# Performance work log

Measured on AMD Instinct MI355X. Metric: run time of the kernel, lower is better.

## Reference

```python
import jax, jax.numpy as jnp
import numpy as np

N, E, B = 20000, 320000, 128      # nodes, edges, graphs in batch
H = 32                            # h_atom == n_bond
N_ATOM_FEAT, N_BOND_FEAT = 64, 16
N_LAYERS = 2


def setup_inputs() -> dict:
    key = jax.random.key(0)
    ks = jax.random.split(key, 12)
    s = 0.1
    return dict(
        n_feat=jax.random.normal(ks[0], (N, N_ATOM_FEAT), jnp.float32),
        e_feat=jax.random.normal(ks[1], (E, N_BOND_FEAT), jnp.float32),
        src=jax.random.randint(ks[2], (E,), 0, N, jnp.int32),
        dst=jax.random.randint(ks[3], (E,), 0, N, jnp.int32),
        graph_ids=jnp.sort(jax.random.randint(ks[4], (N,), 0, B, jnp.int32)),
        W_atom=jax.random.normal(ks[5], (N_ATOM_FEAT, H), jnp.float32) * s,
        b_atom=jnp.zeros((H,), jnp.float32),
        W_bond=jax.random.normal(ks[6], (N_BOND_FEAT, H), jnp.float32) * s,
        b_bond=jnp.zeros((H,), jnp.float32),
        W_e1=jax.random.normal(ks[7], (H, H), jnp.float32) * s,
        b_e1=jnp.zeros((H,), jnp.float32),
        W_e2=jax.random.normal(ks[8], (H, H * H), jnp.float32) * s,
        b_e2=jnp.zeros((H * H,), jnp.float32),
        W_ih=jax.random.normal(ks[9], (3 * H, H), jnp.float32) * s,
        W_hh=jax.random.normal(ks[10], (3 * H, H), jnp.float32) * s,
        b_ih=jnp.zeros((3 * H,), jnp.float32),
        b_hh=jnp.zeros((3 * H,), jnp.float32),
    )


def _gru_step(x, h, W_ih, W_hh, b_ih, b_hh):
    # torch nn.GRU single-cell update (seq_len=1)
    gi = x @ W_ih.T + b_ih
    gh = h @ W_hh.T + b_hh
    ir, iz, ig = jnp.split(gi, 3, axis=-1)
    hr, hz, hg = jnp.split(gh, 3, axis=-1)
    r = jax.nn.sigmoid(ir + hr)
    z = jax.nn.sigmoid(iz + hz)
    n = jnp.tanh(ig + r * hg)
    return (1.0 - z) * n + z * h


def reference(n_feat, e_feat, src, dst, graph_ids, W_atom, b_atom, W_bond, b_bond,
              W_e1, b_e1, W_e2, b_e2, W_ih, W_hh, b_ih, b_hh):
    # dense embeddings
    h = n_feat @ W_atom + b_atom              # [N, H]
    h_bond = e_feat @ W_bond + b_bond         # [E, H]
    # NNConv edge network -> per-edge weight matrix [E, H_in, H_out]
    ew = jax.nn.relu(h_bond @ W_e1 + b_e1) @ W_e2 + b_e2
    W_edge = ew.reshape(E, H, H)
    # in-degree for mean aggregation (zero in-degree -> 0, like DGL mean)
    deg = jax.ops.segment_sum(jnp.ones((E,), h.dtype), dst, num_segments=N)
    inv_deg = 1.0 / jnp.maximum(deg, 1.0)
    for _ in range(N_LAYERS):
        msg = jnp.einsum('ei,eio->eo', h[src], W_edge)                  # [E, H]
        agg = jax.ops.segment_sum(msg, dst, num_segments=N) * inv_deg[:, None]
        m = jax.nn.relu(agg)
        h = _gru_step(m, h, W_ih, W_hh, b_ih, b_hh)
    # dgl.mean_nodes: per-graph mean of node states
    gsum = jax.ops.segment_sum(h, graph_ids, num_segments=B)            # [B, H]
    gcnt = jax.ops.segment_sum(jnp.ones((N,), h.dtype), graph_ids, num_segments=B)
    return gsum / jnp.maximum(gcnt, 1.0)[:, None]
```

## Files before the change

kernel.cpp:

```cpp
#include <hip/hip_runtime.h>
#include <hip/hip_fp16.h>
#include <math.h>

#define N_NODES 20000
#define N_EDGES 320000
#define NB 128
#define H 32
#define AF 64
#define BF 16
#define SCB 79
#define SCP 20224
#define EMB_BLOCKS 2500
#define PACK_BLOCKS 66
#define ZERO_BLOCKS 16

typedef _Float16 f16x2 __attribute__((ext_vector_type(2)));

__device__ __forceinline__ float fast_sigmoid(float x) {
  return 1.0f / (1.0f + __expf(-x));
}
__device__ __forceinline__ float fast_tanh(float x) {
  float e2 = __expf(2.0f * x);
  return 1.0f - 2.0f / (e2 + 1.0f);
}
__device__ __forceinline__ unsigned int pk2(float a, float b) {
  union { f16x2 h; unsigned int u; } p;
  p.h[0] = (_Float16)a;
  p.h[1] = (_Float16)b;
  return p.u;
}
__device__ __forceinline__ float uph(unsigned int u, int hi) {
  union { unsigned int u; f16x2 h; } x; x.u = u;
  return hi ? (float)x.h[1] : (float)x.h[0];
}
__device__ __forceinline__ float dot2(unsigned int a, unsigned int b, float c) {
  union { unsigned int u; f16x2 h; } ua, ub;
  ua.u = a; ub.u = b;
#if __has_builtin(__builtin_amdgcn_fdot2)
  return __builtin_amdgcn_fdot2(ua.h, ub.h, c, false);
#else
  return c + (float)ua.h[0] * (float)ub.h[0] + (float)ua.h[1] * (float)ub.h[1];
#endif
}

__global__ __launch_bounds__(256) void prep(const float* __restrict__ nf,
    const float* __restrict__ W, const float* __restrict__ b, float* __restrict__ h,
    const float* __restrict__ We2, const float* __restrict__ be2,
    unsigned int* __restrict__ Wp, int* __restrict__ hist2buf) {
  int blk = blockIdx.x;
  int tid = threadIdx.x;
  if (blk < EMB_BLOCKS) {
    __shared__ float Ws[AF * H];
    __shared__ float nfs[8][AF];
    for (int v = tid; v < AF * H; v += 256) Ws[v] = W[v];
    int n0 = blk * 8;
    for (int v = tid; v < 8 * AF; v += 256) {
      int nl = v / AF, k = v % AF;
      nfs[nl][k] = nf[(size_t)(n0 + nl) * AF + k];
    }
    __syncthreads();
    int nl = tid / H, o = tid % H;
    int n = n0 + nl;
    float acc = b[o];
#pragma unroll
    for (int k = 0; k < AF; k++) acc += nfs[nl][k] * Ws[k * H + o];
    h[(size_t)n * H + o] = acc;
  } else if (blk < EMB_BLOCKS + PACK_BLOCKS) {
    int idx = (blk - EMB_BLOCKS) * 256 + tid;
    if (idx < 33 * 512) {
      int j = idx >> 9, r = idx & 511;
      int ip = r >> 5, o = r & 31;
      const float* src = (j < 32) ? (We2 + (size_t)j * (H * H)) : be2;
      Wp[idx] = pk2(src[(2 * ip) * H + o], src[(2 * ip + 1) * H + o]);
    }
  } else {
    int idx = (blk - EMB_BLOCKS - PACK_BLOCKS) * 256 + tid;
    for (int i = idx; i < 2 * N_NODES; i += ZERO_BLOCKS * 256) hist2buf[i] = 0;
  }
}

__global__ void hist2(const int* __restrict__ src, const int* __restrict__ dst,
                      int* __restrict__ hsrc, int* __restrict__ hdst) {
  int e = blockIdx.x * 256 + threadIdx.x;
  if (e < N_EDGES) {
    atomicAdd(&hsrc[src[e]], 1);
    atomicAdd(&hdst[dst[e]], 1);
  }
}

__global__ __launch_bounds__(256) void scan_partial(const int* __restrict__ hist_s,
    const int* __restrict__ hist_d, int* __restrict__ part, int* __restrict__ bsum) {
  __shared__ int wsums[4];
  int which = blockIdx.y;
  const int* __restrict__ hh = which ? hist_d : hist_s;
  int i = blockIdx.x * 256 + threadIdx.x;
  int v = (i < N_NODES) ? hh[i] : 0;
  int lane = threadIdx.x & 63, wid = threadIdx.x >> 6;
  int incl = v;
#pragma unroll
  for (int off = 1; off < 64; off <<= 1) {
    int t = __shfl_up(incl, off, 64);
    if (lane >= off) incl += t;
  }
  if (lane == 63) wsums[wid] = incl;
  __syncthreads();
  int woff = 0;
#pragma unroll
  for (int w = 0; w < 4; w++) if (w < wid) woff += wsums[w];
  part[which * SCP + i] = woff + incl - v;
  if (threadIdx.x == 0)
    bsum[which * SCB + blockIdx.x] = wsums[0] + wsums[1] + wsums[2] + wsums[3];
}

__global__ __launch_bounds__(256) void scan_tops(int* __restrict__ bsum,
    const int* __restrict__ gid, int* __restrict__ gstart) {
  __shared__ int s[2 * SCB];
  int tid = threadIdx.x;
  if (tid < 2 * SCB) s[tid] = bsum[tid];
  if (tid < NB) {
    int g = tid;
    int lo = 0, hi = N_NODES;
    while (lo < hi) { int mid = (lo + hi) >> 1; if (gid[mid] < g) lo = mid + 1; else hi = mid; }
    gstart[g] = lo;
    if (g == 0) gstart[NB] = N_NODES;
  }
  __syncthreads();
  if (tid < 2) {
    int run = 0;
    for (int b = 0; b < SCB; b++) { int t = s[tid * SCB + b]; s[tid * SCB + b] = run; run += t; }
  }
  __syncthreads();
  if (tid < 2 * SCB) bsum[tid] = s[tid];
}

__global__ __launch_bounds__(256) void scan_final(const int* __restrict__ part,
    const int* __restrict__ bsum, const int* __restrict__ hist_d,
    int* __restrict__ cur_s, int* __restrict__ cur_d,
    int* __restrict__ seg_s, int* __restrict__ seg_d, float* __restrict__ inv_deg) {
  int which = blockIdx.y;
  int i = blockIdx.x * 256 + threadIdx.x;
  if (i >= N_NODES) return;
  int ex = part[which * SCP + i] + bsum[which * SCB + blockIdx.x];
  if (which == 0) {
    cur_s[i] = ex; seg_s[i] = ex;
    if (i == 0) seg_s[N_NODES] = N_EDGES;
  } else {
    cur_d[i] = ex; seg_d[i] = ex;
    inv_deg[i] = 1.0f / fmaxf((float)hist_d[i], 1.0f);
    if (i == 0) seg_d[N_NODES] = N_EDGES;
  }
}

__global__ void scatter2_full(const int* __restrict__ src, const int* __restrict__ dst,
    int* __restrict__ cur_s, int* __restrict__ cur_d,
    int* __restrict__ src_s, int* __restrict__ dst_s,
    int* __restrict__ pos_s, int* __restrict__ dpos) {
  int e = blockIdx.x * 256 + threadIdx.x;
  if (e >= N_EDGES) return;
  int s = src[e], d = dst[e];
  int ps = atomicAdd(&cur_s[s], 1);
  int pd = atomicAdd(&cur_d[d], 1);
  src_s[ps] = s;
  dst_s[ps] = d;
  dpos[ps] = pd;
  pos_s[e] = ps;
}

__device__ __forceinline__ uint2 edge_r_core(const float* __restrict__ ef,
    const float* __restrict__ Wb, const float* __restrict__ bb,
    const float* __restrict__ We1, const float* __restrict__ be1,
    float* Wbs, unsigned int* W1p, float* efs, unsigned int* hbp,
    int e0, int tid) {
  for (int v = tid; v < BF * H; v += 256) Wbs[v] = Wb[v];
  for (int v = tid; v < 16 * H; v += 256) {
    int jp = v >> 5, o = v & 31;
    W1p[v] = pk2(We1[(2 * jp) * H + o], We1[(2 * jp + 1) * H + o]);
  }
  if (tid < 128) {
    float4 d = ((const float4*)(ef + (size_t)e0 * BF))[tid];
    ((float4*)(efs + (tid >> 2) * 20))[tid & 3] = d;
  }
  __syncthreads();
  int el = tid >> 3, oq = tid & 7;
  const float4* Wb4 = (const float4*)Wbs;
  const float4* efv = (const float4*)(efs + el * 20);
  float4 hb = ((const float4*)bb)[oq];
#pragma unroll
  for (int kq = 0; kq < 4; kq++) {
    float4 e4 = efv[kq];
    float4 w;
    w = Wb4[(kq * 4 + 0) * 8 + oq];
    hb.x += e4.x * w.x; hb.y += e4.x * w.y; hb.z += e4.x * w.z; hb.w += e4.x * w.w;
    w = Wb4[(kq * 4 + 1) * 8 + oq];
    hb.x += e4.y * w.x; hb.y += e4.y * w.y; hb.z += e4.y * w.z; hb.w += e4.y * w.w;
    w = Wb4[(kq * 4 + 2) * 8 + oq];
    hb.x += e4.z * w.x; hb.y += e4.z * w.y; hb.z += e4.z * w.z; hb.w += e4.z * w.w;
    w = Wb4[(kq * 4 + 3) * 8 + oq];
    hb.x += e4.w * w.x; hb.y += e4.w * w.y; hb.z += e4.w * w.z; hb.w += e4.w * w.w;
  }
  ((uint2*)(hbp + el * 20))[oq] = make_uint2(pk2(hb.x, hb.y), pk2(hb.z, hb.w));
  __syncthreads();
  float4 acc = ((const float4*)be1)[oq];
  const uint4* hb4 = (const uint4*)(hbp + el * 20);
#pragma unroll
  for (int q = 0; q < 4; q++) {
    uint4 hp = hb4[q];
    uint4 w;
    w = ((const uint4*)(W1p + (4 * q + 0) * H))[oq];
    acc.x = dot2(hp.x, w.x, acc.x); acc.y = dot2(hp.x, w.y, acc.y);
    acc.z = dot2(hp.x, w.z, acc.z); acc.w = dot2(hp.x, w.w, acc.w);
    w = ((const uint4*)(W1p + (4 * q + 1) * H))[oq];
    acc.x = dot2(hp.y, w.x, acc.x); acc.y = dot2(hp.y, w.y, acc.y);
    acc.z = dot2(hp.y, w.z, acc.z); acc.w = dot2(hp.y, w.w, acc.w);
    w = ((const uint4*)(W1p + (4 * q + 2) * H))[oq];
    acc.x = dot2(hp.z, w.x, acc.x); acc.y = dot2(hp.z, w.y, acc.y);
    acc.z = dot2(hp.z, w.z, acc.z); acc.w = dot2(hp.z, w.w, acc.w);
    w = ((const uint4*)(W1p + (4 * q + 3) * H))[oq];
    acc.x = dot2(hp.w, w.x, acc.x); acc.y = dot2(hp.w, w.y, acc.y);
    acc.z = dot2(hp.w, w.z, acc.z); acc.w = dot2(hp.w, w.w, acc.w);
  }
  acc.x = fmaxf(acc.x, 0.0f); acc.y = fmaxf(acc.y, 0.0f);
  acc.z = fmaxf(acc.z, 0.0f); acc.w = fmaxf(acc.w, 0.0f);
  uint2 st;
  st.x = pk2(acc.x, acc.y);
  st.y = pk2(acc.z, acc.w);
  return st;
}

__global__ __launch_bounds__(256) void edge_r_scatter(const float* __restrict__ ef,
    const float* __restrict__ Wb, const float* __restrict__ bb,
    const float* __restrict__ We1, const float* __restrict__ be1,
    const int* __restrict__ src, const int* __restrict__ dst,
    int* __restrict__ cur_s, int* __restrict__ cur_d,
    int* __restrict__ dpos, unsigned int* __restrict__ rh) {
  __shared__ float Wbs[BF * H];
  __shared__ unsigned int W1p[16 * H];
  __shared__ float efs[32 * 20];
  __shared__ unsigned int hbp[32 * 20];
  __shared__ int psh[32];
  int tid = threadIdx.x;
  int e0 = blockIdx.x * 32;
  int ps0 = 0, pd0 = 0;
  if (tid < 32) {
    int e = e0 + tid;
    int s = src[e], d = dst[e];
    ps0 = atomicAdd(&cur_s[s], 1);
    pd0 = atomicAdd(&cur_d[d], 1);
  }
  for (int v = tid; v < BF * H; v += 256) Wbs[v] = Wb[v];
  for (int v = tid; v < 16 * H; v += 256) {
    int jp = v >> 5, o = v & 31;
    W1p[v] = pk2(We1[(2 * jp) * H + o], We1[(2 * jp + 1) * H + o]);
  }
  if (tid < 128) {
    float4 d = ((const float4*)(ef + (size_t)e0 * BF))[tid];
    ((float4*)(efs + (tid >> 2) * 20))[tid & 3] = d;
  }
  __syncthreads();
  int el = tid >> 3, oq = tid & 7;
  const float4* Wb4 = (const float4*)Wbs;
  const float4* efv = (const float4*)(efs + el * 20);
  float4 hb = ((const float4*)bb)[oq];
#pragma unroll
  for (int kq = 0; kq < 4; kq++) {
    float4 e4 = efv[kq];
    float4 w;
    w = Wb4[(kq * 4 + 0) * 8 + oq];
    hb.x += e4.x * w.x; hb.y += e4.x * w.y; hb.z += e4.x * w.z; hb.w += e4.x * w.w;
    w = Wb4[(kq * 4 + 1) * 8 + oq];
    hb.x += e4.y * w.x; hb.y += e4.y * w.y; hb.z += e4.y * w.z; hb.w += e4.y * w.w;
    w = Wb4[(kq * 4 + 2) * 8 + oq];
    hb.x += e4.z * w.x; hb.y += e4.z * w.y; hb.z += e4.z * w.z; hb.w += e4.z * w.w;
    w = Wb4[(kq * 4 + 3) * 8 + oq];
    hb.x += e4.w * w.x; hb.y += e4.w * w.y; hb.z += e4.w * w.z; hb.w += e4.w * w.w;
  }
  ((uint2*)(hbp + el * 20))[oq] = make_uint2(pk2(hb.x, hb.y), pk2(hb.z, hb.w));
  if (tid < 32) {
    dpos[ps0] = pd0;
    psh[tid] = ps0;
  }
  __syncthreads();
  float4 acc = ((const float4*)be1)[oq];
  const uint4* hb4 = (const uint4*)(hbp + el * 20);
#pragma unroll
  for (int q = 0; q < 4; q++) {
    uint4 hp = hb4[q];
    uint4 w;
    w = ((const uint4*)(W1p + (4 * q + 0) * H))[oq];
    acc.x = dot2(hp.x, w.x, acc.x); acc.y = dot2(hp.x, w.y, acc.y);
    acc.z = dot2(hp.x, w.z, acc.z); acc.w = dot2(hp.x, w.w, acc.w);
    w = ((const uint4*)(W1p + (4 * q + 1) * H))[oq];
    acc.x = dot2(hp.y, w.x, acc.x); acc.y = dot2(hp.y, w.y, acc.y);
    acc.z = dot2(hp.y, w.z, acc.z); acc.w = dot2(hp.y, w.w, acc.w);
    w = ((const uint4*)(W1p + (4 * q + 2) * H))[oq];
    acc.x = dot2(hp.z, w.x, acc.x); acc.y = dot2(hp.z, w.y, acc.y);
    acc.z = dot2(hp.z, w.z, acc.z); acc.w = dot2(hp.z, w.w, acc.w);
    w = ((const uint4*)(W1p + (4 * q + 3) * H))[oq];
    acc.x = dot2(hp.w, w.x, acc.x); acc.y = dot2(hp.w, w.y, acc.y);
    acc.z = dot2(hp.w, w.z, acc.z); acc.w = dot2(hp.w, w.w, acc.w);
  }
  acc.x = fmaxf(acc.x, 0.0f); acc.y = fmaxf(acc.y, 0.0f);
  acc.z = fmaxf(acc.z, 0.0f); acc.w = fmaxf(acc.w, 0.0f);
  int ps = psh[el];
  uint2 st;
  st.x = pk2(acc.x, acc.y);
  st.y = pk2(acc.z, acc.w);
  ((uint2*)(rh + (size_t)ps * 16))[oq] = st;
}

__global__ __launch_bounds__(256) void edge_r(const float* __restrict__ ef,
    const float* __restrict__ Wb, const float* __restrict__ bb,
    const float* __restrict__ We1, const float* __restrict__ be1,
    const int* __restrict__ pos_s, unsigned int* __restrict__ rh) {
  __shared__ float Wbs[BF * H];
  __shared__ unsigned int W1p[16 * H];
  __shared__ float efs[32 * 20];
  __shared__ unsigned int hbp[32 * 20];
  int tid = threadIdx.x;
  int e0 = blockIdx.x * 32;
  uint2 st = edge_r_core(ef, Wb, bb, We1, be1, Wbs, W1p, efs, hbp, e0, tid);
  int el = tid >> 3, oq = tid & 7;
  int ps = pos_s[e0 + el];
  ((uint2*)(rh + (size_t)ps * 16))[oq] = st;
}

__device__ __forceinline__ void msg_phase(const unsigned int* __restrict__ Wp,
    const unsigned int* __restrict__ rh, const int* __restrict__ dpos,
    unsigned int* __restrict__ msg_out,
    unsigned int* Ts, const unsigned int* hp, float* hb, const int* sseg, int tid) {
  {
    int jp = tid >> 4, oh = tid & 15;
    uint2 w0[16], w1[16];
    const unsigned int* W0 = Wp + (size_t)(2 * jp) * 512 + 2 * oh;
    const unsigned int* W1 = Wp + (size_t)(2 * jp + 1) * 512 + 2 * oh;
#pragma unroll
    for (int ip = 0; ip < 16; ip++) {
      w0[ip] = *(const uint2*)(W0 + ip * 32);
      w1[ip] = *(const uint2*)(W1 + ip * 32);
    }
#pragma unroll
    for (int nl = 0; nl < 8; nl++) {
      uint4 h0 = ((const uint4*)(hp + nl * 16))[0];
      uint4 h1 = ((const uint4*)(hp + nl * 16))[1];
      uint4 h2 = ((const uint4*)(hp + nl * 16))[2];
      uint4 h3 = ((const uint4*)(hp + nl * 16))[3];
      unsigned int hr[16] = {h0.x, h0.y, h0.z, h0.w, h1.x, h1.y, h1.z, h1.w,
                             h2.x, h2.y, h2.z, h2.w, h3.x, h3.y, h3.z, h3.w};
      float t00 = 0.f, t01 = 0.f, t10 = 0.f, t11 = 0.f;
#pragma unroll
      for (int ip = 0; ip < 16; ip++) {
        unsigned int hpv = hr[ip];
        t00 = dot2(hpv, w0[ip].x, t00);
        t01 = dot2(hpv, w0[ip].y, t01);
        t10 = dot2(hpv, w1[ip].x, t10);
        t11 = dot2(hpv, w1[ip].y, t11);
      }
      ((uint2*)(Ts + nl * 512 + jp * 32 + 2 * oh))[0] =
          make_uint2(pk2(t00, t10), pk2(t01, t11));
    }
  }
  {
    int nl = tid >> 5, o = tid & 31;
    const unsigned int* Wb32 = Wp + (size_t)32 * 512 + o;
    float acc = 0.f;
#pragma unroll
    for (int ip = 0; ip < 16; ip++)
      acc = dot2(hp[nl * 16 + ip], Wb32[ip * 32], acc);
    hb[nl * H + o] = acc;
  }
  __syncthreads();
  int lane = tid & 63, wid = tid >> 6;
  int el = lane >> 3, t = lane & 7;
  for (int s = 0; s < 8; s++) {
    int a = sseg[s], bnd = sseg[s + 1];
    int ww = (wid + s) & 3;
    if (a + ww * 8 >= bnd) continue;
    const unsigned int* Trow = Ts + s * 512;
    uint4 tw[16];
#pragma unroll
    for (int jp = 0; jp < 16; jp++) tw[jp] = ((const uint4*)(Trow + jp * 32))[t];
    float4 hbv = ((const float4*)(hb + s * H))[t];
    for (int base = a + ww * 8; base < bnd; base += 32) {
      int e = base + el;
      bool valid = (e < bnd);
      int pd = 0;
      unsigned int rr[16];
#pragma unroll
      for (int k = 0; k < 16; k++) rr[k] = 0u;
      if (valid) {
        pd = dpos[e];
        const uint4* rp = (const uint4*)(rh + (size_t)e * 16);
        *(uint4*)(&rr[0])  = rp[0];
        *(uint4*)(&rr[4])  = rp[1];
        *(uint4*)(&rr[8])  = rp[2];
        *(uint4*)(&rr[12]) = rp[3];
      }
      float4 acc = hbv;
#pragma unroll
      for (int jp = 0; jp < 16; jp++) {
        unsigned int rj = rr[jp];
        uint4 w = tw[jp];
        acc.x = dot2(rj, w.x, acc.x);
        acc.y = dot2(rj, w.y, acc.y);
        acc.z = dot2(rj, w.z, acc.z);
        acc.w = dot2(rj, w.w, acc.w);
      }
      if (valid) {
        uint2 st;
        st.x = pk2(acc.x, acc.y);
        st.y = pk2(acc.z, acc.w);
        ((uint2*)(msg_out + (size_t)pd * 16))[t] = st;
      }
    }
  }
}

__global__ __launch_bounds__(256) void edge_msg_T(const float* __restrict__ h,
    const unsigned int* __restrict__ Wp, const unsigned int* __restrict__ rh,
    const int* __restrict__ seg_s, const int* __restrict__ dpos,
    unsigned int* __restrict__ msg_h) {
  __shared__ unsigned int Ts[8 * 512];
  __shared__ unsigned int hp[8 * 16];
  __shared__ float hb[8 * H];
  __shared__ int sseg[9];
  int tid = threadIdx.x;
  int n0 = blockIdx.x * 8;
  if (tid < 128) {
    int nl = tid >> 4, ip = tid & 15;
    float2 hv = ((const float2*)(h + (size_t)(n0 + nl) * H))[ip];
    hp[nl * 16 + ip] = pk2(hv.x, hv.y);
  }
  if (tid < 9) sseg[tid] = seg_s[n0 + tid];
  __syncthreads();
  msg_phase(Wp, rh, dpos, msg_h, Ts, hp, hb, sseg, tid);
}

__global__ __launch_bounds__(256) void gru_msg(const unsigned int* __restrict__ msg_in,
    const int* __restrict__ seg_d, const float* __restrict__ invdeg,
    const float* __restrict__ Wih, const float* __restrict__ Whh,
    const float* __restrict__ bih, const float* __restrict__ bhh,
    float* __restrict__ h,
    const unsigned int* __restrict__ Wp, const unsigned int* __restrict__ rh,
    const int* __restrict__ seg_s, const int* __restrict__ dpos,
    unsigned int* __restrict__ msg_out) {
  __shared__ __align__(16) char smem_u[8 * 512 * 4];
  unsigned int* Wisp = (unsigned int*)smem_u;
  unsigned int* Whsp = Wisp + 96 * 18;
  unsigned int* Ts   = (unsigned int*)smem_u;
  __shared__ unsigned int xpk[8 * 18];
  __shared__ unsigned int hpk[8 * 18];
  __shared__ unsigned int hp[8 * 16];
  __shared__ float hb[8 * H];
  __shared__ int sseg[9];
  int tid = threadIdx.x;
  int n0 = blockIdx.x * 8;
  for (int v = tid; v < 96 * 16; v += 256) {
    int k = v >> 4, ip = v & 15;
    float2 wi = ((const float2*)Wih)[v];
    float2 wh = ((const float2*)Whh)[v];
    Wisp[k * 18 + ip] = pk2(wi.x, wi.y);
    Whsp[k * 18 + ip] = pk2(wh.x, wh.y);
  }
  if (tid < 9) sseg[tid] = seg_s[n0 + tid];
  int node = tid >> 5, o = tid & 31;
  int n = n0 + node;
  int a = seg_d[n], bseg = seg_d[n + 1];
  int q = o & 3, g = o >> 2;
  float acc[8];
#pragma unroll
  for (int k = 0; k < 8; k++) acc[k] = 0.0f;
  int nrows = bseg - a;
#pragma unroll 2
  for (int p = g; p < nrows; p += 8) {
    uint4 m = ((const uint4*)(msg_in + (size_t)(a + p) * 16))[q];
    acc[0] += uph(m.x, 0); acc[1] += uph(m.x, 1);
    acc[2] += uph(m.y, 0); acc[3] += uph(m.y, 1);
    acc[4] += uph(m.z, 0); acc[5] += uph(m.z, 1);
    acc[6] += uph(m.w, 0); acc[7] += uph(m.w, 1);
  }
#pragma unroll
  for (int k = 0; k < 8; k++) {
    acc[k] += __shfl_xor(acc[k], 4, 32);
    acc[k] += __shfl_xor(acc[k], 8, 32);
    acc[k] += __shfl_xor(acc[k], 16, 32);
  }
  float idg = invdeg[n];
  if (g == 0) {
#pragma unroll
    for (int t = 0; t < 4; t++) {
      float xa = fmaxf(acc[2 * t] * idg, 0.0f);
      float xb = fmaxf(acc[2 * t + 1] * idg, 0.0f);
      xpk[node * 18 + 4 * q + t] = pk2(xa, xb);
    }
  }
  float hval = h[(size_t)n * H + o];
  float hnb = __shfl_xor(hval, 1, 32);
  if (!(o & 1)) hpk[node * 18 + (o >> 1)] = pk2(hval, hnb);
  __syncthreads();
  float gi0 = bih[o], gi1 = bih[H + o], gi2 = bih[2 * H + o];
  float gh0 = bhh[o], gh1 = bhh[H + o], gh2 = bhh[2 * H + o];
  {
    const uint2* xr  = (const uint2*)(xpk + node * 18);
    const uint2* hr  = (const uint2*)(hpk + node * 18);
    const uint2* wi0 = (const uint2*)(Wisp + o * 18);
    const uint2* wi1 = (const uint2*)(Wisp + (H + o) * 18);
    const uint2* wi2 = (const uint2*)(Wisp + (2 * H + o) * 18);
    const uint2* wh0 = (const uint2*)(Whsp + o * 18);
    const uint2* wh1 = (const uint2*)(Whsp + (H + o) * 18);
    const uint2* wh2 = (const uint2*)(Whsp + (2 * H + o) * 18);
#pragma unroll
    for (int t = 0; t < 8; t++) {
      uint2 xv = xr[t], hv = hr[t];
      uint2 a0 = wi0[t], a1 = wi1[t], a2 = wi2[t];
      uint2 b0 = wh0[t], b1 = wh1[t], b2 = wh2[t];
      gi0 = dot2(xv.x, a0.x, gi0); gi0 = dot2(xv.y, a0.y, gi0);
      gi1 = dot2(xv.x, a1.x, gi1); gi1 = dot2(xv.y, a1.y, gi1);
      gi2 = dot2(xv.x, a2.x, gi2); gi2 = dot2(xv.y, a2.y, gi2);
      gh0 = dot2(hv.x, b0.x, gh0); gh0 = dot2(hv.y, b0.y, gh0);
      gh1 = dot2(hv.x, b1.x, gh1); gh1 = dot2(hv.y, b1.y, gh1);
      gh2 = dot2(hv.x, b2.x, gh2); gh2 = dot2(hv.y, b2.y, gh2);
    }
  }
  float rg = fast_sigmoid(gi0 + gh0);
  float zg = fast_sigmoid(gi1 + gh1);
  float ng = fast_tanh(gi2 + rg * gh2);
  float hnew = (1.0f - zg) * ng + zg * hval;
  h[(size_t)n * H + o] = hnew;
  float hnb2 = __shfl_xor(hnew, 1, 32);
  if (!(o & 1)) hp[node * 16 + (o >> 1)] = pk2(hnew, hnb2);
  __syncthreads();
  msg_phase(Wp, rh, dpos, msg_out, Ts, hp, hb, sseg, tid);
}

__global__ __launch_bounds__(256) void seg_gru(const unsigned int* __restrict__ msg_h,
    const int* __restrict__ seg_d, const float* __restrict__ invdeg,
    const float* __restrict__ Wih, const float* __restrict__ Whh,
    const float* __restrict__ bih, const float* __restrict__ bhh,
    float* __restrict__ h) {
  __shared__ unsigned int Wisp[96 * 18];
  __shared__ unsigned int Whsp[96 * 18];
  __shared__ unsigned int xpk[8 * 18];
  __shared__ unsigned int hpk[8 * 18];
  int tid = threadIdx.x;
  for (int v = tid; v < 96 * 16; v += 256) {
    int k = v >> 4, ip = v & 15;
    float2 wi = ((const float2*)Wih)[v];
    float2 wh = ((const float2*)Whh)[v];
    Wisp[k * 18 + ip] = pk2(wi.x, wi.y);
    Whsp[k * 18 + ip] = pk2(wh.x, wh.y);
  }
  int node = tid >> 5, o = tid & 31;
  int n = blockIdx.x * 8 + node;
  int a = seg_d[n], bseg = seg_d[n + 1];
  int q = o & 3, g = o >> 2;
  float acc[8];
#pragma unroll
  for (int k = 0; k < 8; k++) acc[k] = 0.0f;
  int nrows = bseg - a;
#pragma unroll 2
  for (int p = g; p < nrows; p += 8) {
    uint4 m = ((const uint4*)(msg_h + (size_t)(a + p) * 16))[q];
    acc[0] += uph(m.x, 0); acc[1] += uph(m.x, 1);
    acc[2] += uph(m.y, 0); acc[3] += uph(m.y, 1);
    acc[4] += uph(m.z, 0); acc[5] += uph(m.z, 1);
    acc[6] += uph(m.w, 0); acc[7] += uph(m.w, 1);
  }
#pragma unroll
  for (int k = 0; k < 8; k++) {
    acc[k] += __shfl_xor(acc[k], 4, 32);
    acc[k] += __shfl_xor(acc[k], 8, 32);
    acc[k] += __shfl_xor(acc[k], 16, 32);
  }
  float idg = invdeg[n];
  if (g == 0) {
#pragma unroll
    for (int t = 0; t < 4; t++) {
      float xa = fmaxf(acc[2 * t] * idg, 0.0f);
      float xb = fmaxf(acc[2 * t + 1] * idg, 0.0f);
      xpk[node * 18 + 4 * q + t] = pk2(xa, xb);
    }
  }
  float hval = h[(size_t)n * H + o];
  float hnb = __shfl_xor(hval, 1, 32);
  if (!(o & 1)) hpk[node * 18 + (o >> 1)] = pk2(hval, hnb);
  __syncthreads();
  float gi0 = bih[o], gi1 = bih[H + o], gi2 = bih[2 * H + o];
  float gh0 = bhh[o], gh1 = bhh[H + o], gh2 = bhh[2 * H + o];
  const uint2* xr  = (const uint2*)(xpk + node * 18);
  const uint2* hr  = (const uint2*)(hpk + node * 18);
  const uint2* wi0 = (const uint2*)(Wisp + o * 18);
  const uint2* wi1 = (const uint2*)(Wisp + (H + o) * 18);
  const uint2* wi2 = (const uint2*)(Wisp + (2 * H + o) * 18);
  const uint2* wh0 = (const uint2*)(Whsp + o * 18);
  const uint2* wh1 = (const uint2*)(Whsp + (H + o) * 18);
  const uint2* wh2 = (const uint2*)(Whsp + (2 * H + o) * 18);
#pragma unroll
  for (int t = 0; t < 8; t++) {
    uint2 xv = xr[t], hv = hr[t];
    uint2 a0 = wi0[t], a1 = wi1[t], a2 = wi2[t];
    uint2 b0 = wh0[t], b1 = wh1[t], b2 = wh2[t];
    gi0 = dot2(xv.x, a0.x, gi0); gi0 = dot2(xv.y, a0.y, gi0);
    gi1 = dot2(xv.x, a1.x, gi1); gi1 = dot2(xv.y, a1.y, gi1);
    gi2 = dot2(xv.x, a2.x, gi2); gi2 = dot2(xv.y, a2.y, gi2);
    gh0 = dot2(hv.x, b0.x, gh0); gh0 = dot2(hv.y, b0.y, gh0);
    gh1 = dot2(hv.x, b1.x, gh1); gh1 = dot2(hv.y, b1.y, gh1);
    gh2 = dot2(hv.x, b2.x, gh2); gh2 = dot2(hv.y, b2.y, gh2);
  }
  float rg = fast_sigmoid(gi0 + gh0);
  float zg = fast_sigmoid(gi1 + gh1);
  float ng = fast_tanh(gi2 + rg * gh2);
  h[(size_t)n * H + o] = (1.0f - zg) * ng + zg * hval;
}

__global__ __launch_bounds__(256) void compute_T_fused(const float* __restrict__ h,
    const unsigned int* __restrict__ Wp,
    unsigned int* __restrict__ Th, float* __restrict__ hbias) {
  __shared__ unsigned int Wall[9 * 512];
  __shared__ unsigned int hp[32 * 17];
  int tid = threadIdx.x;
  int n0 = blockIdx.x * 32;
  int jb = blockIdx.y;
  int nslice = (jb == 3) ? 9 : 8;
  const uint4* Wsrc = (const uint4*)(Wp + (size_t)jb * 8 * 512);
#pragma unroll
  for (int v = 0; v < 4; v++) ((uint4*)Wall)[tid + v * 256] = Wsrc[tid + v * 256];
  if (jb == 3 && tid < 128)
    ((uint4*)(Wall + 8 * 512))[tid] = ((const uint4*)(Wp + 32 * 512))[tid];
  for (int v = tid; v < 512; v += 256) {
    int nl = v >> 4, ip = v & 15;
    float2 hv = ((const float2*)(h + (size_t)(n0 + nl) * H))[ip];
    hp[nl * 17 + ip] = pk2(hv.x, hv.y);
  }
  __syncthreads();
  int nl = tid >> 3, oq = tid & 7;
  unsigned int hreg[16];
#pragma unroll
  for (int ip = 0; ip < 16; ip++) hreg[ip] = hp[nl * 17 + ip];
  int n = n0 + nl;
  float4 pacc = make_float4(0.f, 0.f, 0.f, 0.f);
  for (int jj = 0; jj < nslice; jj++) {
    const uint4* W4 = (const uint4*)(Wall + jj * 512);
    float4 acc = make_float4(0.f, 0.f, 0.f, 0.f);
#pragma unroll
    for (int ip = 0; ip < 16; ip++) {
      unsigned int hpv = hreg[ip];
      uint4 w = W4[ip * 8 + oq];
      acc.x = dot2(hpv, w.x, acc.x);
      acc.y = dot2(hpv, w.y, acc.y);
      acc.z = dot2(hpv, w.z, acc.z);
      acc.w = dot2(hpv, w.w, acc.w);
    }
    int j = jb * 8 + jj;
    if (j < H) {
      if (jj & 1) {
        uint4 st;
        st.x = pk2(pacc.x, acc.x);
        st.y = pk2(pacc.y, acc.y);
        st.z = pk2(pacc.z, acc.z);
        st.w = pk2(pacc.w, acc.w);
        ((uint4*)(Th + (size_t)n * 512 + (j >> 1) * 32))[oq] = st;
      } else {
        pacc = acc;
      }
    } else {
      ((float4*)(hbias + (size_t)n * H))[oq] = acc;
    }
  }
}

__global__ __launch_bounds__(256) void edge_msg_atomic(const unsigned int* __restrict__ rh,
    const unsigned int* __restrict__ Th, const float* __restrict__ hbias,
    const int* __restrict__ src_s, const int* __restrict__ dst_s,
    float* __restrict__ agg) {
  int tid = threadIdx.x;
  int e0 = blockIdx.x * 32;
  int el = tid >> 3, t = tid & 7;
  int e = e0 + el;
  int s = src_s[e], d = dst_s[e];
  uint2 ru2 = ((const uint2*)(rh + (size_t)e * 16))[t];
  float4 acc = ((const float4*)(hbias + (size_t)s * H))[t];
  const unsigned int* Trow = Th + (size_t)s * 512;
#pragma unroll
  for (int jp = 0; jp < 16; jp++) {
    unsigned int mine = (jp & 1) ? ru2.y : ru2.x;
    unsigned int rj = (unsigned int)__shfl((int)mine, jp >> 1, 8);
    uint4 tw = ((const uint4*)(Trow + jp * 32))[t];
    acc.x = dot2(rj, tw.x, acc.x);
    acc.y = dot2(rj, tw.y, acc.y);
    acc.z = dot2(rj, tw.z, acc.z);
    acc.w = dot2(rj, tw.w, acc.w);
  }
  float* ap = agg + (size_t)d * H + t * 4;
  atomicAdd(ap + 0, acc.x);
  atomicAdd(ap + 1, acc.y);
  atomicAdd(ap + 2, acc.z);
  atomicAdd(ap + 3, acc.w);
}

__global__ __launch_bounds__(256) void gru_update(const float* __restrict__ agg,
    const float* __restrict__ invdeg, const float* __restrict__ Wih,
    const float* __restrict__ Whh, const float* __restrict__ bih,
    const float* __restrict__ bhh, float* __restrict__ h) {
  __shared__ float Wis[3 * H][H + 1];
  __shared__ float Whs[3 * H][H + 1];
  __shared__ float xs[8][H + 1];
  __shared__ float hsm[8][H + 1];
  int tid = threadIdx.x;
  for (int v = tid; v < 3 * H * H; v += 256) {
    int k = v / H, i = v % H;
    Wis[k][i] = Wih[v];
    Whs[k][i] = Whh[v];
  }
  int node = tid >> 5, o = tid & 31;
  int n = blockIdx.x * 8 + node;
  xs[node][o] = fmaxf(agg[(size_t)n * H + o] * invdeg[n], 0.0f);
  float hval = h[(size_t)n * H + o];
  hsm[node][o] = hval;
  __syncthreads();
  float gi0 = bih[o], gi1 = bih[H + o], gi2 = bih[2 * H + o];
  float gh0 = bhh[o], gh1 = bhh[H + o], gh2 = bhh[2 * H + o];
#pragma unroll
  for (int i = 0; i < H; i++) {
    float xi = xs[node][i], hi_ = hsm[node][i];
    gi0 += xi * Wis[o][i];
    gh0 += hi_ * Whs[o][i];
    gi1 += xi * Wis[H + o][i];
    gh1 += hi_ * Whs[H + o][i];
    gi2 += xi * Wis[2 * H + o][i];
    gh2 += hi_ * Whs[2 * H + o][i];
  }
  float rg = fast_sigmoid(gi0 + gh0);
  float zg = fast_sigmoid(gi1 + gh1);
  float ng = fast_tanh(gi2 + rg * gh2);
  h[(size_t)n * H + o] = (1.0f - zg) * ng + zg * hval;
}

__global__ __launch_bounds__(256) void readout_graph(const float* __restrict__ h,
    const int* __restrict__ gstart, float* __restrict__ out) {
  __shared__ float red[8][H + 1];
  int g = blockIdx.x;
  int a = gstart[g], b = gstart[g + 1];
  int r = threadIdx.x >> 5, o = threadIdx.x & 31;
  float s = 0.0f;
  for (int n = a + r; n < b; n += 8) s += h[(size_t)n * H + o];
  red[r][o] = s;
  __syncthreads();
  if (r == 0) {
    float t = 0.0f;
#pragma unroll
    for (int k = 0; k < 8; k++) t += red[k][o];
    out[g * H + o] = t / fmaxf((float)(b - a), 1.0f);
  }
}

extern "C" void kernel_launch(void* const* d_in, const int* in_sizes, int n_in,
                              void* d_out, int out_size, void* d_ws, size_t ws_size,
                              hipStream_t stream) {
  const float* n_feat = (const float*)d_in[0];
  const float* e_feat = (const float*)d_in[1];
  const int*   src    = (const int*)d_in[2];
  const int*   dst    = (const int*)d_in[3];
  const int*   gid    = (const int*)d_in[4];
  const float* W_atom = (const float*)d_in[5];
  const float* b_atom = (const float*)d_in[6];
  const float* W_bond = (const float*)d_in[7];
  const float* b_bond = (const float*)d_in[8];
  const float* W_e1   = (const float*)d_in[9];
  const float* b_e1   = (const float*)d_in[10];
  const float* W_e2   = (const float*)d_in[11];
  const float* b_e2   = (const float*)d_in[12];
  const float* W_ih   = (const float*)d_in[13];
  const float* W_hh   = (const float*)d_in[14];
  const float* b_ih   = (const float*)d_in[15];
  const float* b_hh   = (const float*)d_in[16];
  float* out = (float*)d_out;

  char* ws = (char*)d_ws;
  size_t off = 0;
  float*        h      = (float*)(ws + off); off += (size_t)N_NODES * H * 4;
  unsigned int* rh     = (unsigned int*)(ws + off); off += (size_t)N_EDGES * 16 * 4;
  unsigned int* Th     = (unsigned int*)(ws + off); off += (size_t)N_NODES * 512 * 4;
  float*        hbias  = (float*)(ws + off); off += (size_t)N_NODES * H * 4;
  unsigned int* Wp     = (unsigned int*)(ws + off); off += (size_t)33 * 512 * 4;
  int*   hist_s = (int*)(ws + off);   off += (size_t)N_NODES * 4;
  int*   hist_d = (int*)(ws + off);   off += (size_t)N_NODES * 4;
  int*   cur_s  = (int*)(ws + off);   off += (size_t)N_NODES * 4;
  int*   cur_d  = (int*)(ws + off);   off += (size_t)N_NODES * 4;
  int*   seg_s  = (int*)(ws + off);   off += (size_t)(N_NODES + 1) * 4;
  int*   seg_d  = (int*)(ws + off);   off += (size_t)(N_NODES + 1) * 4;
  float* invdeg = (float*)(ws + off); off += (size_t)N_NODES * 4;
  int*   part   = (int*)(ws + off);   off += (size_t)2 * SCP * 4;
  int*   bsum   = (int*)(ws + off);   off += (size_t)2 * SCB * 4;
  int*   src_s  = (int*)(ws + off);   off += (size_t)N_EDGES * 4;
  int*   dst_s  = (int*)(ws + off);   off += (size_t)N_EDGES * 4;
  int*   dpos   = (int*)(ws + off);   off += (size_t)N_EDGES * 4;
  int*   gstart = (int*)(ws + off);   off += (size_t)(NB + 1) * 4;
  float* agg    = (float*)(ws + off); off += (size_t)N_NODES * H * 4;
  unsigned int* msg_h  = (unsigned int*)(ws + off); off += (size_t)N_EDGES * 16 * 4;
  unsigned int* msg_h2 = (unsigned int*)(ws + off); off += (size_t)N_EDGES * 16 * 4;
  int use_msg = (ws_size >= off) ? 1 : 0;
  int* pos_s = (int*)Th;

  prep<<<EMB_BLOCKS + PACK_BLOCKS + ZERO_BLOCKS, 256, 0, stream>>>(
      n_feat, W_atom, b_atom, h, W_e2, b_e2, Wp, hist_s);

  hist2<<<(N_EDGES + 255) / 256, 256, 0, stream>>>(src, dst, hist_s, hist_d);
  {
    dim3 gs(SCB, 2);
    scan_partial<<<gs, 256, 0, stream>>>(hist_s, hist_d, part, bsum);
    scan_tops<<<1, 256, 0, stream>>>(bsum, gid, gstart);
    scan_final<<<gs, 256, 0, stream>>>(part, bsum, hist_d, cur_s, cur_d,
                                       seg_s, seg_d, invdeg);
  }

  if (use_msg) {
    edge_r_scatter<<<N_EDGES / 32, 256, 0, stream>>>(e_feat, W_bond, b_bond,
                                                     W_e1, b_e1, src, dst,
                                                     cur_s, cur_d, dpos, rh);
    edge_msg_T<<<N_NODES / 8, 256, 0, stream>>>(h, Wp, rh, seg_s, dpos, msg_h);
    gru_msg<<<N_NODES / 8, 256, 0, stream>>>(msg_h, seg_d, invdeg,
                                             W_ih, W_hh, b_ih, b_hh, h,
                                             Wp, rh, seg_s, dpos, msg_h2);
    seg_gru<<<N_NODES / 8, 256, 0, stream>>>(msg_h2, seg_d, invdeg,
                                             W_ih, W_hh, b_ih, b_hh, h);
  } else {
    scatter2_full<<<(N_EDGES + 255) / 256, 256, 0, stream>>>(src, dst, cur_s, cur_d,
                                                             src_s, dst_s, pos_s, dpos);
    edge_r<<<N_EDGES / 32, 256, 0, stream>>>(e_feat, W_bond, b_bond, W_e1, b_e1,
                                             pos_s, rh);
    for (int layer = 0; layer < 2; layer++) {
      dim3 gT(N_NODES / 32, 4);
      compute_T_fused<<<gT, 256, 0, stream>>>(h, Wp, Th, hbias);
      hipMemsetAsync(agg, 0, (size_t)N_NODES * H * 4, stream);
      edge_msg_atomic<<<N_EDGES / 32, 256, 0, stream>>>(rh, Th, hbias, src_s, dst_s,
                                                        agg);
      gru_update<<<N_NODES / 8, 256, 0, stream>>>(agg, invdeg,
                                                  W_ih, W_hh, b_ih, b_hh, h);
    }
  }

  readout_graph<<<NB, 256, 0, stream>>>(h, gstart, out);
}
```

Measured before the change: 274.5 us.

## Assign one source node per wave and prefetch next edge batch in registers

Changes the edge-message loop so each of the four waves owns two fixed source nodes instead of every wave striding over all eight. Within a node the wave walks its edges eight at a time, loading the next batch's row data and destination index into registers while computing the current one. The aim is to hide global-load latency and cut the per-node weight-tile reloads. The cost is more register pressure and possible imbalance between waves when nodes have uneven out-degree.

New measurement: 277.0 us. Within noise of the previous version (+0.9%).

```diff
diff --git a/kernel.cpp b/kernel.cpp
--- a/kernel.cpp
+++ b/kernel.cpp
@@ -371,30 +371,37 @@
   __syncthreads();
   int lane = tid & 63, wid = tid >> 6;
   int el = lane >> 3, t = lane & 7;
-  for (int s = 0; s < 8; s++) {
+#pragma unroll
+  for (int si = 0; si < 2; si++) {
+    int s = wid + si * 4;
     int a = sseg[s], bnd = sseg[s + 1];
-    int ww = (wid + s) & 3;
-    if (a + ww * 8 >= bnd) continue;
+    if (a >= bnd) continue;
     const unsigned int* Trow = Ts + s * 512;
     uint4 tw[16];
 #pragma unroll
     for (int jp = 0; jp < 16; jp++) tw[jp] = ((const uint4*)(Trow + jp * 32))[t];
     float4 hbv = ((const float4*)(hb + s * H))[t];
-    for (int base = a + ww * 8; base < bnd; base += 32) {
-      int e = base + el;
-      bool valid = (e < bnd);
-      int pd = 0;
-      unsigned int rr[16];
-#pragma unroll
-      for (int k = 0; k < 16; k++) rr[k] = 0u;
-      if (valid) {
-        pd = dpos[e];
-        const uint4* rp = (const uint4*)(rh + (size_t)e * 16);
-        *(uint4*)(&rr[0])  = rp[0];
-        *(uint4*)(&rr[4])  = rp[1];
-        *(uint4*)(&rr[8])  = rp[2];
-        *(uint4*)(&rr[12]) = rp[3];
+    int e = a + el;
+    bool valid = (e < bnd);
+    int pd = 0;
+    uint4 r0 = make_uint4(0u,0u,0u,0u), r1 = r0, r2 = r0, r3 = r0;
+    if (valid) {
+      pd = dpos[e];
+      const uint4* rp = (const uint4*)(rh + (size_t)e * 16);
+      r0 = rp[0]; r1 = rp[1]; r2 = rp[2]; r3 = rp[3];
+    }
+    for (int base = a; base < bnd; base += 8) {
+      int e2 = base + 8 + el;
+      bool v2 = (base + 8 < bnd) && (e2 < bnd);
+      int pd2 = 0;
+      uint4 n0 = make_uint4(0u,0u,0u,0u), n1 = n0, n2 = n0, n3 = n0;
+      if (v2) {
+        pd2 = dpos[e2];
+        const uint4* rp = (const uint4*)(rh + (size_t)e2 * 16);
+        n0 = rp[0]; n1 = rp[1]; n2 = rp[2]; n3 = rp[3];
       }
+      unsigned int rr[16] = {r0.x, r0.y, r0.z, r0.w, r1.x, r1.y, r1.z, r1.w,
+                             r2.x, r2.y, r2.z, r2.w, r3.x, r3.y, r3.z, r3.w};
       float4 acc = hbv;
 #pragma unroll
       for (int jp = 0; jp < 16; jp++) {
@@ -411,6 +418,8 @@
         st.y = pk2(acc.z, acc.w);
         ((uint2*)(msg_out + (size_t)pd * 16))[t] = st;
       }
+      valid = v2; pd = pd2;
+      r0 = n0; r1 = n1; r2 = n2; r3 = n3;
     }
   }
 }
```
